# Kernel optimization log

Measured on AMD Instinct MI355X. Metric: run time of the kernel, lower is better.

## Reference

```python
import jax, jax.numpy as jnp
import numpy as np

BN_EPS = 1e-5


def setup_inputs() -> dict:
    key = jax.random.key(0)
    ks = jax.random.split(key, 10)
    d = {}
    # EEG-style input: [B, 1, T, electrodes]
    d["x"] = jax.random.normal(ks[0], (512, 1, 1125, 5), dtype=jnp.float32)
    # conv_time: Conv2d(1, 40, (25, 1)) with bias
    d["conv_time_w"] = jax.random.normal(ks[1], (40, 1, 25, 1), dtype=jnp.float32) * 0.05
    d["conv_time_b"] = jax.random.normal(ks[2], (40,), dtype=jnp.float32) * 0.05
    # conv_spat: Conv2d(40, 40, (1, 5), bias=False)
    d["conv_spat_w"] = jax.random.normal(ks[3], (40, 40, 1, 5), dtype=jnp.float32) * 0.05
    # BatchNorm2d(40), eval mode (running stats)
    d["bn_gamma"] = jnp.ones((40,), jnp.float32)
    d["bn_beta"] = jnp.zeros((40,), jnp.float32)
    d["bn_mean"] = jnp.zeros((40,), jnp.float32)
    d["bn_var"] = jnp.ones((40,), jnp.float32)
    # LSTM(input=40, hidden=10): torch layout W_ih [4H, in], W_hh [4H, H]
    d["w_ih"] = jax.random.normal(ks[4], (40, 40), dtype=jnp.float32) * 0.1
    d["w_hh"] = jax.random.normal(ks[5], (40, 10), dtype=jnp.float32) * 0.1
    d["b_ih"] = jax.random.normal(ks[6], (40,), dtype=jnp.float32) * 0.1
    d["b_hh"] = jax.random.normal(ks[7], (40,), dtype=jnp.float32) * 0.1
    # classifier: Linear(10, 2)
    d["fc_w"] = jax.random.normal(ks[8], (2, 10), dtype=jnp.float32) * 0.1
    d["fc_b"] = jnp.zeros((2,), jnp.float32)
    return d


def reference(x, conv_time_w, conv_time_b, conv_spat_w,
              bn_gamma, bn_beta, bn_mean, bn_var,
              w_ih, w_hh, b_ih, b_hh, fc_w, fc_b):
    dn = ("NCHW", "OIHW", "NCHW")
    # conv over time: [B,1,T,5] -> [B,40,T-24,5]
    h = jax.lax.conv_general_dilated(x, conv_time_w, (1, 1), "VALID", dimension_numbers=dn)
    h = h + conv_time_b[None, :, None, None]
    # conv over electrodes: [B,40,T-24,5] -> [B,40,T-24,1]
    h = jax.lax.conv_general_dilated(h, conv_spat_w, (1, 1), "VALID", dimension_numbers=dn)
    # BatchNorm2d (eval, running stats)
    scale = bn_gamma / jnp.sqrt(bn_var + BN_EPS)
    h = h * scale[None, :, None, None] + (bn_beta - bn_mean * scale)[None, :, None, None]
    # AvgPool2d kernel (25,1) stride (5,1): -> [B,40,L,1], L = (T-24-25)//5 + 1
    h = jax.lax.reduce_window(h, 0.0, jax.lax.add, (1, 1, 25, 1), (1, 1, 5, 1), "VALID") / 25.0
    # Dropout2d in eval mode = identity
    # squeeze width + transpose(1,2): [B,40,L] -> [B,L,40]
    h = jnp.transpose(h[..., 0], (0, 2, 1))
    B = h.shape[0]
    H = w_hh.shape[1]  # hidden = 10
    # precompute input-to-gate projection for all timesteps: [L, B, 4H]
    xg = jnp.einsum("blf,gf->lbg", h, w_ih) + b_ih + b_hh

    def step(carry, xt):
        h_prev, c_prev = carry
        gates = xt + h_prev @ w_hh.T          # [B, 4H]
        i, f, g, o = jnp.split(gates, 4, axis=-1)
        i = jax.nn.sigmoid(i)
        f = jax.nn.sigmoid(f)
        g = jnp.tanh(g)
        o = jax.nn.sigmoid(o)
        c = f * c_prev + i * g
        hn = o * jnp.tanh(c)
        return (hn, c), None

    init = (jnp.zeros((B, H), h.dtype), jnp.zeros((B, H), h.dtype))
    (h_last, _), _ = jax.lax.scan(step, init, xg)  # return_seq=False -> last hidden
    return h_last @ fc_w.T + fc_b  # [B, 2]
```

## Files before the change

kernel.cpp:

```cpp
#include <hip/hip_runtime.h>

#define LOG2E 1.44269504088896340736f

typedef float v2f __attribute__((ext_vector_type(2)));

__device__ __forceinline__ float bf2f(unsigned short u) {
    union { unsigned u32; float f; } v; v.u32 = ((unsigned)u) << 16; return v.f;
}
__device__ __forceinline__ unsigned short f2bf(float f) {
    union { float f; unsigned u32; } v; v.f = f;
    unsigned r = (v.u32 + 0x7FFFu + ((v.u32 >> 16) & 1u)) >> 16;
    return (unsigned short)r;
}
__device__ __forceinline__ bool probe_bf16(const void* gma) {
    return *(const unsigned int*)gma == 0x3F803F80u;
}
__device__ __forceinline__ float ldmix(const void* p, int i, bool bf) {
    return bf ? bf2f(((const unsigned short*)p)[i]) : ((const float*)p)[i];
}
__device__ __forceinline__ float dpp_shl(float x, const int n) {
    int r;
    if (n == 1)      r = __builtin_amdgcn_update_dpp(0, __float_as_int(x), 0x101, 0xF, 0xF, true);
    else if (n == 2) r = __builtin_amdgcn_update_dpp(0, __float_as_int(x), 0x102, 0xF, 0xF, true);
    else             r = __builtin_amdgcn_update_dpp(0, __float_as_int(x), 0x103, 0xF, 0xF, true);
    return __int_as_float(r);
}

__global__ __launch_bounds__(1024) void prep_kernel(
    const void* __restrict__ ctw,
    const void* __restrict__ ctb,
    const void* __restrict__ csw,
    const void* __restrict__ gma,
    const void* __restrict__ bta,
    const void* __restrict__ mea,
    const void* __restrict__ var,
    const void* __restrict__ wih,
    const void* __restrict__ bih,
    const void* __restrict__ bhh,
    float* __restrict__ Wg,
    float* __restrict__ Bg)
{
    __shared__ float s_wt[1000];
    __shared__ float s_bt[40];
    __shared__ float s_sp[8000];
    __shared__ float s_wih[1600];
    __shared__ float s_scale[40], s_shift[40];
    __shared__ float s_Wc[5000];
    __shared__ float s_P[5200];
    __shared__ float s_Bc[40];
    __shared__ float s_Wp[9920];

    const int t = threadIdx.x;
    const bool bf = probe_bf16(gma);

    for (int i = t; i < 1000; i += 1024) s_wt[i] = ldmix(ctw, i, bf);
    for (int i = t; i < 8000; i += 1024) s_sp[i] = ldmix(csw, i, bf);
    for (int i = t; i < 1600; i += 1024) s_wih[i] = ldmix(wih, i, bf);
    if (t < 40) {
        s_bt[t] = ldmix(ctb, t, bf);
        float sc = ldmix(gma, t, bf) * rsqrtf(ldmix(var, t, bf) + 1e-5f);
        s_scale[t] = sc;
        s_shift[t] = ldmix(bta, t, bf) - ldmix(mea, t, bf) * sc;
    }
    __syncthreads();

    if (t < 200) {
        const int oc = t / 5, kq = (t % 5) * 5;
        float acc[5][5];
        #pragma unroll
        for (int q = 0; q < 5; ++q)
            #pragma unroll
            for (int e = 0; e < 5; ++e) acc[q][e] = 0.f;
        for (int ic = 0; ic < 40; ++ic) {
            float wtv[5], spv[5];
            #pragma unroll
            for (int q = 0; q < 5; ++q) wtv[q] = s_wt[ic * 25 + kq + q];
            #pragma unroll
            for (int e = 0; e < 5; ++e) spv[e] = s_sp[(oc * 40 + ic) * 5 + e];
            #pragma unroll
            for (int q = 0; q < 5; ++q)
                #pragma unroll
                for (int e = 0; e < 5; ++e) acc[q][e] = fmaf(wtv[q], spv[e], acc[q][e]);
        }
        const float sc = s_scale[oc];
        #pragma unroll
        for (int q = 0; q < 5; ++q)
            #pragma unroll
            for (int e = 0; e < 5; ++e)
                s_Wc[(oc * 25 + kq + q) * 5 + e] = acc[q][e] * sc;
    }
    if (t >= 512 && t < 552) {
        const int oc = t - 512;
        float a = 0.f;
        for (int ic = 0; ic < 40; ++ic) {
            float se = 0.f;
            #pragma unroll
            for (int e = 0; e < 5; ++e) se += s_sp[(oc * 40 + ic) * 5 + e];
            a = fmaf(se, s_bt[ic], a);
        }
        s_Bc[oc] = a * s_scale[oc] + s_shift[oc];
    }
    __syncthreads();

    if (t < 200) {
        const int oc = t / 5, e = t % 5;
        float run = 0.f;
        s_P[oc * 130 + e] = 0.f;
        for (int k = 0; k < 25; ++k) {
            run += s_Wc[(oc * 25 + k) * 5 + e];
            s_P[oc * 130 + (k + 1) * 5 + e] = run;
        }
    }
    __syncthreads();

    for (int i = t; i < 9800; i += 1024) {
        const int oc = i / 245, rem = i % 245, j = rem / 5, e = rem % 5;
        const int lo = j - 24 > 0 ? j - 24 : 0;
        const int hi = j < 24 ? j : 24;
        float val = (s_P[oc * 130 + (hi + 1) * 5 + e] - s_P[oc * 130 + lo * 5 + e]) * 0.04f;
        s_Wp[oc * 248 + rem] = val;
    }
    if (t < 120) s_Wp[(t / 3) * 248 + 245 + (t % 3)] = 0.f;
    __syncthreads();

    if (t < 620) {
        const int gp = t / 31, ko = t % 31;
        const int g0 = 2 * gp, kf0 = 8 * ko;
        float acc0[8], acc1[8];
        #pragma unroll
        for (int q = 0; q < 8; ++q) { acc0[q] = 0.f; acc1[q] = 0.f; }
        for (int oc = 0; oc < 40; ++oc) {
            const float4 pa = *reinterpret_cast<const float4*>(&s_Wp[oc * 248 + kf0]);
            const float4 pb = *reinterpret_cast<const float4*>(&s_Wp[oc * 248 + kf0 + 4]);
            const float wa = s_wih[g0 * 40 + oc];
            const float wb = s_wih[(g0 + 1) * 40 + oc];
            acc0[0] = fmaf(wa, pa.x, acc0[0]); acc0[1] = fmaf(wa, pa.y, acc0[1]);
            acc0[2] = fmaf(wa, pa.z, acc0[2]); acc0[3] = fmaf(wa, pa.w, acc0[3]);
            acc0[4] = fmaf(wa, pb.x, acc0[4]); acc0[5] = fmaf(wa, pb.y, acc0[5]);
            acc0[6] = fmaf(wa, pb.z, acc0[6]); acc0[7] = fmaf(wa, pb.w, acc0[7]);
            acc1[0] = fmaf(wb, pa.x, acc1[0]); acc1[1] = fmaf(wb, pa.y, acc1[1]);
            acc1[2] = fmaf(wb, pa.z, acc1[2]); acc1[3] = fmaf(wb, pa.w, acc1[3]);
            acc1[4] = fmaf(wb, pb.x, acc1[4]); acc1[5] = fmaf(wb, pb.y, acc1[5]);
            acc1[6] = fmaf(wb, pb.z, acc1[6]); acc1[7] = fmaf(wb, pb.w, acc1[7]);
        }
        #pragma unroll
        for (int q = 0; q < 8; ++q) {
            Wg[g0 * 248 + kf0 + q]       = acc0[q];
            Wg[(g0 + 1) * 248 + kf0 + q] = acc1[q];
        }
    }
    if (t >= 640 && t < 680) {
        const int g = t - 640;
        float a = ldmix(bih, g, bf) + ldmix(bhh, g, bf);
        for (int oc = 0; oc < 40; ++oc) a = fmaf(s_wih[g * 40 + oc], s_Bc[oc], a);
        Bg[g] = a;
    }
}

__global__ __launch_bounds__(256, 2) void fused_kernel(
    const void* __restrict__ x,
    const float* __restrict__ Wg,
    const float* __restrict__ Bg,
    const void* __restrict__ whh_p,
    const void* __restrict__ fcw_p,
    const void* __restrict__ fcb_p,
    const void* __restrict__ gma,
    void* __restrict__ out)
{
    __shared__ float u[8960];

    const int b   = blockIdx.x;
    const int tid = threadIdx.x;
    const bool bf = probe_bf16(gma);

    if (bf) {
        const unsigned short* xp = (const unsigned short*)x + b * 5625;
        for (int i = tid; i < 5625; i += 256) u[i] = bf2f(xp[i]);
    } else {
        const float* xp = (const float*)x + b * 5625;
        for (int i = tid; i < 5625; i += 256) u[i] = xp[i];
    }
    for (int i = 5625 + tid; i < 6144; i += 256) u[i] = 0.f;
    for (int i = 8640 + tid; i < 8960; i += 256) u[i] = 0.f;
    __syncthreads();

    const int wave  = __builtin_amdgcn_readfirstlane(tid >> 6);
    const int lane  = tid & 63;
    const int gb    = 20 * (wave & 1);
    const int lbase = 108 * (wave >> 1);
    const int l0 = lbase + lane;
    const int l1 = l0 + 64;
    const int a0 = 25 * l0, a1 = 25 * l1;

    v2f acc[20];
    #pragma unroll
    for (int gi = 0; gi < 20; ++gi) {
        float bgv = Bg[gb + gi];
        acc[gi] = (v2f){bgv, bgv};
    }

    const float* wp = Wg + gb * 248;
    float4 wa[20], wb[20];
    #pragma unroll
    for (int gi = 0; gi < 20; ++gi)
        wa[gi] = *reinterpret_cast<const float4*>(wp + gi * 248);

    for (int k = 0; k < 248; k += 8) {
        #pragma unroll
        for (int gi = 0; gi < 20; ++gi)
            wb[gi] = *reinterpret_cast<const float4*>(wp + gi * 248 + k + 4);
        {
            v2f xv[4];
            #pragma unroll
            for (int kk = 0; kk < 4; ++kk)
                xv[kk] = (v2f){ u[a0 + k + kk], u[a1 + k + kk] };
            #pragma unroll
            for (int gi = 0; gi < 20; ++gi) {
                acc[gi] += xv[0] * wa[gi].x;
                acc[gi] += xv[1] * wa[gi].y;
                acc[gi] += xv[2] * wa[gi].z;
                acc[gi] += xv[3] * wa[gi].w;
            }
        }
        #pragma unroll
        for (int gi = 0; gi < 20; ++gi)
            wa[gi] = *reinterpret_cast<const float4*>(wp + gi * 248 + k + 8);
        {
            v2f xv[4];
            #pragma unroll
            for (int kk = 0; kk < 4; ++kk)
                xv[kk] = (v2f){ u[a0 + k + 4 + kk], u[a1 + k + 4 + kk] };
            #pragma unroll
            for (int gi = 0; gi < 20; ++gi) {
                acc[gi] += xv[0] * wb[gi].x;
                acc[gi] += xv[1] * wb[gi].y;
                acc[gi] += xv[2] * wb[gi].z;
                acc[gi] += xv[3] * wb[gi].w;
            }
        }
    }
    __syncthreads();

    #pragma unroll
    for (int gi = 0; gi < 20; ++gi) {
        u[l0 * 40 + gb + gi] = acc[gi].x;
        if (lane < 44) u[l1 * 40 + gb + gi] = acc[gi].y;
    }
    __syncthreads();

    if (wave != 0) return;

    const int j   = lane >> 2;
    const int jt  = lane & 3;
    const int jj  = j < 10 ? j : 9;
    const int gl  = 10 * jt + jj;

    float whhr[10];
    #pragma unroll
    for (int m = 0; m < 10; ++m) whhr[m] = ldmix(whh_p, gl * 10 + m, bf);

    const float kmul = (jt == 2) ?  2.0f * LOG2E : -LOG2E;
    const float aact = (jt == 2) ? -2.0f : 1.0f;
    const float bact = (jt == 2) ?  1.0f : 0.0f;

    float xb[6];
    #pragma unroll
    for (int p = 0; p < 6; ++p) xb[p] = u[p * 40 + gl];

    float c = 0.f, h = 0.f;

    for (int l = 0; l < 216; l += 6) {
        #pragma unroll
        for (int s = 0; s < 6; ++s) {
            float xv = xb[s];
            xb[s] = u[(l + s + 6) * 40 + gl];
            float a_ = xv, b_ = 0.f;
            #pragma unroll
            for (int m = 0; m < 10; m += 2) {
                float h0 = __int_as_float(__builtin_amdgcn_readlane(__float_as_int(h), 4 * m));
                float h1 = __int_as_float(__builtin_amdgcn_readlane(__float_as_int(h), 4 * (m + 1)));
                a_ = fmaf(whhr[m], h0, a_);
                b_ = fmaf(whhr[m + 1], h1, b_);
            }
            float accg = a_ + b_;
            float tt  = exp2f(kmul * accg);
            float rr  = __builtin_amdgcn_rcpf(1.0f + tt);
            float act = fmaf(aact, rr, bact);
            float fv = dpp_shl(act, 1);
            float gv = dpp_shl(act, 2);
            float ov = dpp_shl(act, 3);
            c = fmaf(fv, c, act * gv);
            float t2 = exp2f(2.0f * LOG2E * c);
            float r2 = __builtin_amdgcn_rcpf(1.0f + t2);
            float th = fmaf(-2.0f, r2, 1.0f);
            h = ov * th;
        }
    }

    float w0[10], w1[10];
    #pragma unroll
    for (int m = 0; m < 10; ++m) {
        w0[m] = ldmix(fcw_p, m, bf);
        w1[m] = ldmix(fcw_p, 10 + m, bf);
    }
    float o0 = ldmix(fcb_p, 0, bf), o1 = ldmix(fcb_p, 1, bf);
    #pragma unroll
    for (int m = 0; m < 10; ++m) {
        float hm = __int_as_float(__builtin_amdgcn_readlane(__float_as_int(h), 4 * m));
        o0 = fmaf(w0[m], hm, o0);
        o1 = fmaf(w1[m], hm, o1);
    }
    if (lane == 0) {
        if (bf) {
            ((unsigned short*)out)[b * 2]     = f2bf(o0);
            ((unsigned short*)out)[b * 2 + 1] = f2bf(o1);
        } else {
            ((float*)out)[b * 2]     = o0;
            ((float*)out)[b * 2 + 1] = o1;
        }
    }
}

extern "C" void kernel_launch(void* const* d_in, const int* in_sizes, int n_in,
                              void* d_out, int out_size, void* d_ws, size_t ws_size,
                              hipStream_t stream) {
    const void* x    = d_in[0];
    const void* ctw  = d_in[1];
    const void* ctb  = d_in[2];
    const void* csw  = d_in[3];
    const void* gma  = d_in[4];
    const void* bta  = d_in[5];
    const void* mea  = d_in[6];
    const void* var  = d_in[7];
    const void* wih  = d_in[8];
    const void* whh  = d_in[9];
    const void* bih  = d_in[10];
    const void* bhh  = d_in[11];
    const void* fcw  = d_in[12];
    const void* fcb  = d_in[13];

    char* ws = (char*)d_ws;
    float* Wg = (float*)ws;
    float* Bg = (float*)(ws + 40 * 248 * 4);

    prep_kernel<<<1, 1024, 0, stream>>>(ctw, ctb, csw, gma, bta, mea, var,
                                        wih, bih, bhh, Wg, Bg);
    fused_kernel<<<512, 256, 0, stream>>>(x, Wg, Bg, whh, fcw, fcb, gma, d_out);
}
```

Baseline: 179.2 us.

## Stage gate weights in LDS and fold activation scales into LSTM weights

The 40x248 combined gate weight matrix is copied into shared memory once per block, and the projection loop reads float4 weights from LDS instead of double-buffered global loads held in registers. This cuts register pressure and global/L1 traffic. The cost is about 39 KB of extra LDS per block, which may limit occupancy. In the LSTM recurrence, the exp2 scale factor is pre-multiplied into the recurrent weights and input gates, and the input gate's activation carries the 2*log2e factor, so the cell state is tracked pre-scaled. Raw v_exp_f32 replaces exp2f, removing multiplies and range handling from the serial critical path.

New measurement: 163.6 us. 1.1x faster.

```diff
diff --git a/kernel.cpp b/kernel.cpp
--- a/kernel.cpp
+++ b/kernel.cpp
@@ -25,6 +25,13 @@
     else             r = __builtin_amdgcn_update_dpp(0, __float_as_int(x), 0x103, 0xF, 0xF, true);
     return __int_as_float(r);
 }
+#if __has_builtin(__builtin_amdgcn_exp2f)
+__device__ __forceinline__ float fexp2(float x) { return __builtin_amdgcn_exp2f(x); }
+#else
+__device__ __forceinline__ float fexp2(float x) {
+    float r; asm("v_exp_f32 %0, %1" : "=v"(r) : "v"(x)); return r;
+}
+#endif
 
 __global__ __launch_bounds__(1024) void prep_kernel(
     const void* __restrict__ ctw,
@@ -167,12 +174,14 @@
     const void* __restrict__ gma,
     void* __restrict__ out)
 {
+    __shared__ float sw[9920];
     __shared__ float u[8960];
 
     const int b   = blockIdx.x;
     const int tid = threadIdx.x;
     const bool bf = probe_bf16(gma);
 
+    for (int i = tid; i < 9920; i += 256) sw[i] = Wg[i];
     if (bf) {
         const unsigned short* xp = (const unsigned short*)x + b * 5625;
         for (int i = tid; i < 5625; i += 256) u[i] = bf2f(xp[i]);
@@ -199,44 +208,19 @@
         acc[gi] = (v2f){bgv, bgv};
     }
 
-    const float* wp = Wg + gb * 248;
-    float4 wa[20], wb[20];
-    #pragma unroll
-    for (int gi = 0; gi < 20; ++gi)
-        wa[gi] = *reinterpret_cast<const float4*>(wp + gi * 248);
-
-    for (int k = 0; k < 248; k += 8) {
-        #pragma unroll
-        for (int gi = 0; gi < 20; ++gi)
-            wb[gi] = *reinterpret_cast<const float4*>(wp + gi * 248 + k + 4);
-        {
-            v2f xv[4];
-            #pragma unroll
-            for (int kk = 0; kk < 4; ++kk)
-                xv[kk] = (v2f){ u[a0 + k + kk], u[a1 + k + kk] };
-            #pragma unroll
-            for (int gi = 0; gi < 20; ++gi) {
-                acc[gi] += xv[0] * wa[gi].x;
-                acc[gi] += xv[1] * wa[gi].y;
-                acc[gi] += xv[2] * wa[gi].z;
-                acc[gi] += xv[3] * wa[gi].w;
-            }
-        }
-        #pragma unroll
-        for (int gi = 0; gi < 20; ++gi)
-            wa[gi] = *reinterpret_cast<const float4*>(wp + gi * 248 + k + 8);
-        {
-            v2f xv[4];
-            #pragma unroll
-            for (int kk = 0; kk < 4; ++kk)
-                xv[kk] = (v2f){ u[a0 + k + 4 + kk], u[a1 + k + 4 + kk] };
-            #pragma unroll
-            for (int gi = 0; gi < 20; ++gi) {
-                acc[gi] += xv[0] * wb[gi].x;
-                acc[gi] += xv[1] * wb[gi].y;
-                acc[gi] += xv[2] * wb[gi].z;
-                acc[gi] += xv[3] * wb[gi].w;
-            }
+    const int wrow = gb * 248;
+    for (int k = 0; k < 248; k += 4) {
+        v2f xv0 = (v2f){ u[a0 + k],     u[a1 + k]     };
+        v2f xv1 = (v2f){ u[a0 + k + 1], u[a1 + k + 1] };
+        v2f xv2 = (v2f){ u[a0 + k + 2], u[a1 + k + 2] };
+        v2f xv3 = (v2f){ u[a0 + k + 3], u[a1 + k + 3] };
+        #pragma unroll
+        for (int gi = 0; gi < 20; ++gi) {
+            const float4 w = *reinterpret_cast<const float4*>(&sw[wrow + gi * 248 + k]);
+            acc[gi] += xv0 * w.x;
+            acc[gi] += xv1 * w.y;
+            acc[gi] += xv2 * w.z;
+            acc[gi] += xv3 * w.w;
         }
     }
     __syncthreads();
@@ -255,25 +239,26 @@
     const int jj  = j < 10 ? j : 9;
     const int gl  = 10 * jt + jj;
 
+    const float L2   = 2.0f * LOG2E;
+    const float kmul = (jt == 2) ?  L2 : -LOG2E;
+    const float aact = (jt == 2) ? -2.0f : (jt == 0 ? L2 : 1.0f);
+    const float bact = (jt == 2) ?  1.0f : 0.0f;
+
     float whhr[10];
     #pragma unroll
-    for (int m = 0; m < 10; ++m) whhr[m] = ldmix(whh_p, gl * 10 + m, bf);
-
-    const float kmul = (jt == 2) ?  2.0f * LOG2E : -LOG2E;
-    const float aact = (jt == 2) ? -2.0f : 1.0f;
-    const float bact = (jt == 2) ?  1.0f : 0.0f;
+    for (int m = 0; m < 10; ++m) whhr[m] = kmul * ldmix(whh_p, gl * 10 + m, bf);
 
     float xb[6];
     #pragma unroll
-    for (int p = 0; p < 6; ++p) xb[p] = u[p * 40 + gl];
-
-    float c = 0.f, h = 0.f;
+    for (int p = 0; p < 6; ++p) xb[p] = kmul * u[p * 40 + gl];
+
+    float cs = 0.f, h = 0.f;
 
     for (int l = 0; l < 216; l += 6) {
         #pragma unroll
         for (int s = 0; s < 6; ++s) {
             float xv = xb[s];
-            xb[s] = u[(l + s + 6) * 40 + gl];
+            xb[s] = kmul * u[(l + s + 6) * 40 + gl];
             float a_ = xv, b_ = 0.f;
             #pragma unroll
             for (int m = 0; m < 10; m += 2) {
@@ -283,14 +268,14 @@
                 b_ = fmaf(whhr[m + 1], h1, b_);
             }
             float accg = a_ + b_;
-            float tt  = exp2f(kmul * accg);
+            float tt  = fexp2(accg);
             float rr  = __builtin_amdgcn_rcpf(1.0f + tt);
             float act = fmaf(aact, rr, bact);
             float fv = dpp_shl(act, 1);
             float gv = dpp_shl(act, 2);
             float ov = dpp_shl(act, 3);
-            c = fmaf(fv, c, act * gv);
-            float t2 = exp2f(2.0f * LOG2E * c);
+            cs = fmaf(fv, cs, act * gv);
+            float t2 = fexp2(cs);
             float r2 = __builtin_amdgcn_rcpf(1.0f + t2);
             float th = fmaf(-2.0f, r2, 1.0f);
             h = ov * th;
```
